# Kernel tuning notes

Hardware: AMD Instinct MI355X
Metric: run time of the kernel (lower is better)

## Reference

```python
import jax, jax.numpy as jnp
import numpy as np

# ---- static config (Phi-3-small layer 0, blocksparse branch) ----
HIDDEN = 4096
N_HEADS = 32
N_KV = 8
HEAD_DIM = HIDDEN // N_HEADS        # 128
Q_PER_KV = N_HEADS // N_KV          # 4
SEQ = 2048
ROPE_BASE = 1000000.0
POS_SCALE = 1.0
SM_SCALE = 1.0 / HEAD_DIM           # mup scaling, multiplier=1.0
BLOCK = 64
LOCAL_BLOCKS = 16
VERT_STRIDE = 8


def _blocksparse_mask(seq_len):
    """Dense [S,S] bool mask realizing the causal blocksparse pattern:
    query block i attends key block j iff j<=i and (i-j < LOCAL_BLOCKS or (j+1) % VERT_STRIDE == 0),
    with elementwise causality inside blocks. Built once in numpy (static)."""
    nb = seq_len // BLOCK
    qb = np.arange(nb)[:, None]
    kb = np.arange(nb)[None, :]
    bmask = (kb <= qb) & ((qb - kb < LOCAL_BLOCKS) | ((kb + 1) % VERT_STRIDE == 0))
    emask = np.kron(bmask, np.ones((BLOCK, BLOCK), dtype=bool))
    i = np.arange(seq_len)
    emask &= i[:, None] >= i[None, :]
    return jnp.asarray(emask)


def _rope(x, cos, sin):
    # x: [B, S, H, D]; cos/sin: [S, D]
    x1, x2 = jnp.split(x, 2, axis=-1)
    rot = jnp.concatenate([-x2, x1], axis=-1)
    return x * cos[None, :, None, :] + rot * sin[None, :, None, :]


def setup_inputs() -> dict:
    key = jax.random.key(0)
    k1, k2, k3, k4, k5 = jax.random.split(key, 5)
    qkv_out = (N_HEADS + 2 * N_KV) * HEAD_DIM  # 6144
    return {
        "hidden_states": jax.random.normal(k1, (1, SEQ, HIDDEN), dtype=jnp.float32),
        "w_qkv": jax.random.normal(k2, (qkv_out, HIDDEN), dtype=jnp.float32) * 0.02,
        "b_qkv": jnp.zeros((qkv_out,), dtype=jnp.float32),
        "w_dense": jax.random.normal(k3, (HIDDEN, HIDDEN), dtype=jnp.float32) * 0.02,
        "b_dense": jnp.zeros((HIDDEN,), dtype=jnp.float32),
    }


def reference(hidden_states, w_qkv, b_qkv, w_dense, b_dense):
    B, S, _ = hidden_states.shape
    # grouped QKV projection: [B,S,(H+2*KV)*D]
    qkv = jnp.einsum("bsh,oh->bso", hidden_states, w_qkv) + b_qkv
    # group layout: (group, q0..q3, k, v) per kv head
    qkv = qkv.reshape(B, S, N_KV, Q_PER_KV + 2, HEAD_DIM)
    q = qkv[:, :, :, :Q_PER_KV].reshape(B, S, N_HEADS, HEAD_DIM)
    k = qkv[:, :, :, Q_PER_KV]   # [B,S,KV,D]
    v = qkv[:, :, :, Q_PER_KV + 1]
    # rotary embeddings (HF rotate-half style)
    inv_freq = 1.0 / (ROPE_BASE ** (jnp.arange(0, HEAD_DIM, 2, dtype=jnp.float32) / HEAD_DIM))
    t = jnp.arange(S, dtype=jnp.float32) * POS_SCALE
    freqs = jnp.outer(t, inv_freq)               # [S, D/2]
    emb = jnp.concatenate([freqs, freqs], axis=-1)
    cos, sin = jnp.cos(emb), jnp.sin(emb)
    q = _rope(q, cos, sin)
    k = _rope(k, cos, sin)
    # GQA: replicate kv heads to match q heads
    k = jnp.repeat(k, Q_PER_KV, axis=2)          # [B,S,H,D]
    v = jnp.repeat(v, Q_PER_KV, axis=2)
    mask = _blocksparse_mask(S)                  # [S,S] bool
    scores = jnp.einsum("bqhd,bkhd->bhqk", q, k) * SM_SCALE
    scores = jnp.where(mask[None, None], scores, jnp.finfo(scores.dtype).min)
    probs = jax.nn.softmax(scores, axis=-1)
    ctx = jnp.einsum("bhqk,bkhd->bqhd", probs, v).reshape(B, S, HIDDEN)
    out = jnp.einsum("bsh,oh->bso", ctx, w_dense) + b_dense
    return out
```

## Files before the change

### kernel.cpp

```cpp
#include <hip/hip_runtime.h>
#include <hip/hip_bf16.h>

#define SEQ 2048
#define HIDDEN 4096
#define NH 32
#define NKV 8
#define HD 128
#define QKV_OUT 6144
#define QSCALE (0.0078125f * 1.4426950408889634f)

typedef __attribute__((ext_vector_type(8))) short bf16x8;
typedef __attribute__((ext_vector_type(4))) float f32x4;
typedef __attribute__((ext_vector_type(16))) float f32x16;

__device__ inline unsigned short f32_bf16(float f) {
  union { float f; unsigned int u; } v; v.f = f;
  unsigned int r = v.u + 0x7FFFu + ((v.u >> 16) & 1u);
  return (unsigned short)(r >> 16);
}
__device__ inline float bf16_f32(unsigned short u) {
  union { unsigned int u; float f; } v; v.u = (unsigned int)u << 16;
  return v.f;
}
__device__ inline unsigned int pk(float a, float b) {
  union { __hip_bfloat162 h; unsigned int u; } t;
  t.h = __float22bfloat162_rn(make_float2(a, b));
  return t.u;
}
__device__ inline void pswap(unsigned int &a, unsigned int &b) {
  auto r = __builtin_amdgcn_permlane32_swap((int)a, (int)b, false, false);
  a = (unsigned int)r[0]; b = (unsigned int)r[1];
}
__device__ inline float xmax32(float v) {
  int x = __builtin_bit_cast(int, v);
  auto r = __builtin_amdgcn_permlane32_swap(x, x, false, false);
  return fmaxf(__builtin_bit_cast(float, (int)r[0]), __builtin_bit_cast(float, (int)r[1]));
}
__device__ inline float xadd32(float v) {
  int x = __builtin_bit_cast(int, v);
  auto r = __builtin_amdgcn_permlane32_swap(x, x, false, false);
  return __builtin_bit_cast(float, (int)r[0]) + __builtin_bit_cast(float, (int)r[1]);
}

__device__ inline void cast8(const float* __restrict__ in, unsigned short* __restrict__ out) {
  float4 a = *reinterpret_cast<const float4*>(in);
  float4 b = *reinterpret_cast<const float4*>(in + 4);
  unsigned short t[8];
  t[0] = f32_bf16(a.x); t[1] = f32_bf16(a.y); t[2] = f32_bf16(a.z); t[3] = f32_bf16(a.w);
  t[4] = f32_bf16(b.x); t[5] = f32_bf16(b.y); t[6] = f32_bf16(b.z); t[7] = f32_bf16(b.w);
  *reinterpret_cast<uint4*>(out) = *reinterpret_cast<uint4*>(t);
}

#define N1 ((size_t)SEQ * HIDDEN / 8)
#define N2 ((size_t)QKV_OUT * HIDDEN / 8)
#define N4 ((size_t)HIDDEN * HIDDEN / 8)
#define N3 ((size_t)SEQ * 64)
__global__ __launch_bounds__(256) void prep(const float* __restrict__ hid,
                                            unsigned short* __restrict__ hid_bf,
                                            const float* __restrict__ wq,
                                            unsigned short* __restrict__ wq_bf,
                                            const float* __restrict__ wd,
                                            unsigned short* __restrict__ wd_bf,
                                            float* __restrict__ ct,
                                            float* __restrict__ st) {
  size_t i = (size_t)blockIdx.x * 256 + threadIdx.x;
  if (i < N1) {
    cast8(hid + i * 8, hid_bf + i * 8);
  } else if (i < N1 + N2) {
    size_t j = (i - N1) * 8;
    cast8(wq + j, wq_bf + j);
  } else if (i < N1 + N2 + N4) {
    size_t j = (i - N1 - N2) * 8;
    cast8(wd + j, wd_bf + j);
  } else {
    size_t j = i - N1 - N2 - N4;
    int s = (int)(j >> 6), d = (int)(j & 63);
    float inv = powf(1.0e6f, -(float)d * (1.0f / 64.0f));
    float f = (float)s * inv;
    ct[j] = cosf(f);
    st[j] = sinf(f);
  }
}

template <int BM, int BN, int CR, int CC, bool OBF>
__global__ __launch_bounds__(512, 2) void gemmG(const unsigned short* __restrict__ A,
                                                const unsigned short* __restrict__ B,
                                                const float* __restrict__ bias,
                                                void* __restrict__ Cp,
                                                int M, int N, int K) {
  constexpr int MQ   = BM / 64;
  constexpr int NREP = BN / 64;
  constexpr int NB0  = (NREP + 1) / 2;
  constexpr int La   = BM / 128;
  constexpr int NB   = BN / 64;
  constexpr int AH   = BM * 64;
  constexpr int SB   = 2 * AH + BN * 128;
  __shared__ __align__(16) char Lds[SB * 2];

  const int tid = threadIdx.x;
  const int wave = tid >> 6, lane = tid & 63;
  const int wr = wave >> 2, wc = wave & 3;
  const int lrow = lane & 15, lgrp = lane >> 4;

  const int ntx = N / BN;
  const int wg0 = blockIdx.x;
  const int xcd = wg0 & 7, w = wg0 >> 3;
  const int cpb = ntx / CC;
  const int band = xcd / cpb, colc = xcd % cpb;
  const int bm = (band * CR + w / CC) * BM;
  const int bn = (colc * CC + w % CC) * BN;

  const int r8 = lane >> 3;
  const int scol = ((lane & 7) ^ r8) * 8;

  const unsigned short* gA[2][La]; int lA[2][La];
#pragma unroll
  for (int u = 0; u < 2; ++u)
#pragma unroll
    for (int j = 0; j < La; ++j) {
      int row = bm + u * (BM / 2) + wave * (BM / 16) + j * 8 + r8;
      gA[u][j] = A + (size_t)row * K + scol;
      lA[u][j] = u * AH + (wave * (BM / 16) + j * 8) * 128;
    }
  const unsigned short* gB[NB]; int lB[NB];
#pragma unroll
  for (int j = 0; j < NB; ++j) {
    int row = bn + wave * (BN / 8) + j * 8 + r8;
    gB[j] = B + (size_t)row * K + scol;
    lB[j] = 2 * AH + (wave * (BN / 8) + j * 8) * 128;
  }

  auto stageA2 = [&](int bufb, int k0) {
#pragma unroll
    for (int u = 0; u < 2; ++u)
#pragma unroll
      for (int j = 0; j < La; ++j)
        __builtin_amdgcn_global_load_lds(
            (const __attribute__((address_space(1))) unsigned int*)(gA[u][j] + k0),
            (__attribute__((address_space(3))) unsigned int*)(Lds + bufb + lA[u][j]), 16, 0, 0);
  };
  auto stageB = [&](int bufb, int k0) {
#pragma unroll
    for (int j = 0; j < NB; ++j)
      __builtin_amdgcn_global_load_lds(
          (const __attribute__((address_space(1))) unsigned int*)(gB[j] + k0),
          (__attribute__((address_space(3))) unsigned int*)(Lds + bufb + lB[j]), 16, 0, 0);
  };

  const int rsw = (lrow & 7) << 4;
  auto aoff = [&](int mh, int m, int ks) {
    int r = mh * (BM / 4) + m * 16 + lrow;
    return wr * AH + r * 128 + ((ks * 64 + lgrp * 16) ^ rsw);
  };
  auto boff = [&](int nf, int ks) {
    int r = wc * (BN / 4) + nf * 16 + lrow;
    return 2 * AH + r * 128 + ((ks * 64 + lgrp * 16) ^ rsw);
  };

  f32x4 acc[2 * MQ][NREP] = {};
  bf16x8 af[MQ][2], bf[NREP][2];

  const int nt = K / 64;
  stageA2(0, 0);
  stageB(0, 0);

  for (int t = 0; t < nt; ++t) {
    const int cur = (t & 1) ? SB : 0;
    const int nxt = cur ^ SB;
    const bool pf = (t + 1) < nt;
    const int k1 = (t + 1) * 64;
    const char* base = Lds + cur;

    if (pf) {
      stageA2(nxt, k1);
      if constexpr (La == 2) asm volatile("s_waitcnt vmcnt(4)" ::: "memory");
      else                   asm volatile("s_waitcnt vmcnt(2)" ::: "memory");
    } else {
      asm volatile("s_waitcnt vmcnt(0)" ::: "memory");
    }
    __builtin_amdgcn_sched_barrier(0);
    __builtin_amdgcn_s_barrier();
    __builtin_amdgcn_sched_barrier(0);
#pragma unroll
    for (int m = 0; m < MQ; ++m)
#pragma unroll
      for (int ks = 0; ks < 2; ++ks)
        af[m][ks] = *reinterpret_cast<const bf16x8*>(base + aoff(0, m, ks));
#pragma unroll
    for (int nf = 0; nf < NB0; ++nf)
#pragma unroll
      for (int ks = 0; ks < 2; ++ks)
        bf[nf][ks] = *reinterpret_cast<const bf16x8*>(base + boff(nf, ks));
    __builtin_amdgcn_s_setprio(1);
#pragma unroll
    for (int m = 0; m < MQ; ++m)
#pragma unroll
      for (int nf = 0; nf < NB0; ++nf)
#pragma unroll
        for (int ks = 0; ks < 2; ++ks)
          acc[m][nf] = __builtin_amdgcn_mfma_f32_16x16x32_bf16(af[m][ks], bf[nf][ks], acc[m][nf], 0, 0, 0);
    __builtin_amdgcn_s_setprio(0);

    if (pf) stageB(nxt, k1);
#pragma unroll
    for (int nf = NB0; nf < NREP; ++nf)
#pragma unroll
      for (int ks = 0; ks < 2; ++ks)
        bf[nf][ks] = *reinterpret_cast<const bf16x8*>(base + boff(nf, ks));
    __builtin_amdgcn_s_setprio(1);
#pragma unroll
    for (int m = 0; m < MQ; ++m)
#pragma unroll
      for (int nf = NB0; nf < NREP; ++nf)
#pragma unroll
        for (int ks = 0; ks < 2; ++ks)
          acc[m][nf] = __builtin_amdgcn_mfma_f32_16x16x32_bf16(af[m][ks], bf[nf][ks], acc[m][nf], 0, 0, 0);
    __builtin_amdgcn_s_setprio(0);

#pragma unroll
    for (int m = 0; m < MQ; ++m)
#pragma unroll
      for (int ks = 0; ks < 2; ++ks)
        af[m][ks] = *reinterpret_cast<const bf16x8*>(base + aoff(1, m, ks));
    __builtin_amdgcn_s_setprio(1);
#pragma unroll
    for (int m = 0; m < MQ; ++m)
#pragma unroll
      for (int nf = 0; nf < NB0; ++nf)
#pragma unroll
        for (int ks = 0; ks < 2; ++ks)
          acc[MQ + m][nf] = __builtin_amdgcn_mfma_f32_16x16x32_bf16(af[m][ks], bf[nf][ks], acc[MQ + m][nf], 0, 0, 0);
    __builtin_amdgcn_s_setprio(0);

    __builtin_amdgcn_s_setprio(1);
#pragma unroll
    for (int m = 0; m < MQ; ++m)
#pragma unroll
      for (int nf = NB0; nf < NREP; ++nf)
#pragma unroll
        for (int ks = 0; ks < 2; ++ks)
          acc[MQ + m][nf] = __builtin_amdgcn_mfma_f32_16x16x32_bf16(af[m][ks], bf[nf][ks], acc[MQ + m][nf], 0, 0, 0);
    __builtin_amdgcn_s_setprio(0);
  }

#pragma unroll
  for (int ni = 0; ni < NREP; ++ni) {
    int col = bn + wc * (BN / 4) + ni * 16 + lrow;
    float bv = bias[col];
#pragma unroll
    for (int mi = 0; mi < 2 * MQ; ++mi)
#pragma unroll
      for (int r = 0; r < 4; ++r) {
        int row = bm + wr * (BM / 2) + mi * 16 + lgrp * 4 + r;
        if constexpr (OBF)
          ((unsigned short*)Cp)[(size_t)row * N + col] = f32_bf16(acc[mi][ni][r] + bv);
        else
          ((float*)Cp)[(size_t)row * N + col] = acc[mi][ni][r] + bv;
      }
  }
}

__global__ __launch_bounds__(256) void rope_split(const unsigned short* __restrict__ qkvb,
                                                  const float* __restrict__ ct,
                                                  const float* __restrict__ st,
                                                  unsigned short* __restrict__ Q,
                                                  unsigned short* __restrict__ Kh,
                                                  unsigned short* __restrict__ Vt) {
  int b = blockIdx.x;
  if (b < 5120) {
    int t = b * 256 + threadIdx.x;
    int d8 = (t & 15) * 8;
    int q = t >> 4;
    int s = q / 40;
    int slotg = q - s * 40;
    int g = slotg / 5, slot = slotg - g * 5;
    const unsigned short* base = qkvb + (size_t)s * QKV_OUT + g * 768 + slot * 128;
    bf16x8 x8 = *reinterpret_cast<const bf16x8*>(base + d8);
    bf16x8 r8 = *reinterpret_cast<const bf16x8*>(base + (d8 ^ 64));
    float4 c0 = *reinterpret_cast<const float4*>(ct + s * 64 + (d8 & 63));
    float4 c1 = *reinterpret_cast<const float4*>(ct + s * 64 + (d8 & 63) + 4);
    float4 s0 = *reinterpret_cast<const float4*>(st + s * 64 + (d8 & 63));
    float4 s1 = *reinterpret_cast<const float4*>(st + s * 64 + (d8 & 63) + 4);
    float cc[8] = {c0.x, c0.y, c0.z, c0.w, c1.x, c1.y, c1.z, c1.w};
    float ss[8] = {s0.x, s0.y, s0.z, s0.w, s1.x, s1.y, s1.z, s1.w};
    float sgn = (d8 < 64) ? -1.0f : 1.0f;
    float sc = (slot < 4) ? QSCALE : 1.0f;
    unsigned short o[8];
#pragma unroll
    for (int i = 0; i < 8; ++i) {
      float x = bf16_f32((unsigned short)x8[i]);
      float r = bf16_f32((unsigned short)r8[i]) * sgn;
      o[i] = f32_bf16((x * cc[i] + r * ss[i]) * sc);
    }
    unsigned short* dst = (slot < 4)
        ? Q + ((size_t)(g * 4 + slot) * SEQ + s) * HD + d8
        : Kh + ((size_t)g * SEQ + s) * HD + d8;
    *reinterpret_cast<uint4*>(dst) = *reinterpret_cast<uint4*>(o);
  } else {
    int t2 = (b - 5120) * 256 + threadIdx.x;
    int d = t2 & 127;
    int rest = t2 >> 7;
    int g = rest & 7;
    int s0 = (rest >> 3) * 8;
    const unsigned short* src = qkvb + (size_t)s0 * QKV_OUT + g * 768 + 640 + d;
    unsigned short o[8];
#pragma unroll
    for (int i = 0; i < 8; ++i) o[i] = src[(size_t)i * QKV_OUT];
    *reinterpret_cast<uint4*>(&Vt[((size_t)g * HD + d) * SEQ + s0]) =
        *reinterpret_cast<uint4*>(o);
  }
}

__device__ inline int nextj(int x, int qb) {
  if (x > qb) return -1;
  if (qb - x < 16) return x;
  int v = (x & ~7) + 7;
  int w = qb - 15;
  return v < w ? v : w;
}

__global__ __launch_bounds__(256, 2) void attn32(const unsigned short* __restrict__ Q,
                                                 const unsigned short* __restrict__ Kh,
                                                 const unsigned short* __restrict__ Vt,
                                                 unsigned short* __restrict__ ctx) {
  const int g = blockIdx.x;
  const int y = (int)gridDim.y - 1 - (int)blockIdx.y;
  const int qb = y >> 1, half = y & 1;
  const int Q0 = y * 32;
  const int tid = threadIdx.x;
  const int wave = tid >> 6;
  const int h = g * 4 + wave;
  const int lane = tid & 63;
  const int l31 = lane & 31, hi = lane >> 5;

  __shared__ __align__(16) char Lds[65536];

  auto stage = [&](int bufb, int j) {
#pragma unroll
    for (int i = 0; i < 4; ++i) {
      int row = i * 16 + (tid >> 4);
      const unsigned short* src =
          Kh + ((size_t)(g * SEQ + j * 64 + row)) * HD + ((tid & 15) ^ (row & 15)) * 8;
      __builtin_amdgcn_global_load_lds(
          (const __attribute__((address_space(1))) unsigned int*)src,
          (__attribute__((address_space(3))) unsigned int*)(Lds + bufb + i * 4096 + (tid >> 6) * 1024),
          16, 0, 0);
    }
#pragma unroll
    for (int i = 0; i < 4; ++i) {
      int row = i * 32 + (tid >> 3);
      const unsigned short* src =
          Vt + ((size_t)(g * HD + row)) * SEQ + j * 64 + ((tid & 7) ^ (row & 7)) * 8;
      __builtin_amdgcn_global_load_lds(
          (const __attribute__((address_space(1))) unsigned int*)src,
          (__attribute__((address_space(3))) unsigned int*)(Lds + bufb + 16384 + i * 4096 + (tid >> 6) * 1024),
          16, 0, 0);
    }
  };

  bf16x8 qf[8];
  const unsigned short* qbase = Q + ((size_t)h * SEQ + Q0 + l31) * HD;
#pragma unroll
  for (int kk = 0; kk < 8; ++kk)
    qf[kk] = *reinterpret_cast<const bf16x8*>(qbase + kk * 16 + hi * 8);

  f32x16 ot[4] = {};
  float mrow = -1e30f, lsum = 0.f;

  const int kswz = l31 & 15;
  const int vswz = l31 & 7;

  int j = nextj(0, qb);
  int cur = 0;
  stage(0, j);
  asm volatile("s_waitcnt vmcnt(0)" ::: "memory");
  __builtin_amdgcn_sched_barrier(0);
  __builtin_amdgcn_s_barrier();
  __builtin_amdgcn_sched_barrier(0);

  while (true) {
    const int jn = (j < qb) ? nextj(j + 1, qb) : -1;
    if (jn >= 0) stage(cur ^ 32768, jn);

    const char* kb = Lds + cur;
    const char* vb = Lds + cur + 16384;
    const bool diag = (j == qb);
    const bool short_blk = diag && (half == 0);

    f32x16 st[2] = {};
    __builtin_amdgcn_s_setprio(1);
#pragma unroll
    for (int kk = 0; kk < 8; ++kk) {
      bf16x8 k0 = *reinterpret_cast<const bf16x8*>(
          kb + (size_t)l31 * 256 + (((2 * kk + hi) ^ kswz) * 16));
      st[0] = __builtin_amdgcn_mfma_f32_32x32x16_bf16(k0, qf[kk], st[0], 0, 0, 0);
      if (!short_blk) {
        bf16x8 k1 = *reinterpret_cast<const bf16x8*>(
            kb + (size_t)(32 + l31) * 256 + (((2 * kk + hi) ^ kswz) * 16));
        st[1] = __builtin_amdgcn_mfma_f32_32x32x16_bf16(k1, qf[kk], st[1], 0, 0, 0);
      }
    }
    __builtin_amdgcn_s_setprio(0);

    if (diag) {
      int qrel = half * 32 + l31;
#pragma unroll
      for (int kt = 0; kt < 2; ++kt)
#pragma unroll
        for (int r = 0; r < 16; ++r) {
          int krel = kt * 32 + (r & 3) + 8 * (r >> 2) + 4 * hi;
          if (krel > qrel) st[kt][r] = -1e30f;
        }
    }

    float t16[16];
#pragma unroll
    for (int r = 0; r < 16; ++r) t16[r] = fmaxf(st[0][r], st[1][r]);
#pragma unroll
    for (int sft = 8; sft >= 1; sft >>= 1)
#pragma unroll
      for (int r = 0; r < sft; ++r) t16[r] = fmaxf(t16[r], t16[r + sft]);
    float vm = xmax32(t16[0]);

    if (!__all(vm - mrow <= 8.0f)) {
      float nm = fmaxf(mrow, vm);
      float corr = __builtin_amdgcn_exp2f(mrow - nm);
      lsum *= corr;
#pragma unroll
      for (int dt = 0; dt < 4; ++dt)
#pragma unroll
        for (int r = 0; r < 16; ++r) ot[dt][r] *= corr;
      mrow = nm;
    }

    float s4[4] = {0.f, 0.f, 0.f, 0.f};
#pragma unroll
    for (int kt = 0; kt < 2; ++kt)
#pragma unroll
      for (int r = 0; r < 16; ++r) {
        float p = __builtin_amdgcn_exp2f(st[kt][r] - mrow);
        st[kt][r] = p;
        s4[r & 3] += p;
      }
    lsum += xadd32((s4[0] + s4[1]) + (s4[2] + s4[3]));

    bf16x8 pb[4];
#pragma unroll
    for (int s = 0; s < 4; ++s) {
      int kt = s >> 1, g0 = (s & 1) * 2, g1 = g0 + 1;
      unsigned int a0 = pk(st[kt][4 * g0 + 0], st[kt][4 * g0 + 1]);
      unsigned int a1 = pk(st[kt][4 * g0 + 2], st[kt][4 * g0 + 3]);
      unsigned int b0 = pk(st[kt][4 * g1 + 0], st[kt][4 * g1 + 1]);
      unsigned int b1 = pk(st[kt][4 * g1 + 2], st[kt][4 * g1 + 3]);
      pswap(a0, b0);
      pswap(a1, b1);
      union { unsigned int u[4]; bf16x8 v; } t;
      t.u[0] = a0; t.u[1] = a1; t.u[2] = b0; t.u[3] = b1;
      pb[s] = t.v;
    }

    const int smax = short_blk ? 2 : 4;
    __builtin_amdgcn_s_setprio(1);
#pragma unroll
    for (int dt = 0; dt < 4; ++dt) {
      const char* vrow = vb + (size_t)(dt * 32 + l31) * 128;
#pragma unroll
      for (int s = 0; s < 4; ++s)
        if (s < smax)
          ot[dt] = __builtin_amdgcn_mfma_f32_32x32x16_bf16(
              *reinterpret_cast<const bf16x8*>(vrow + (((2 * s + hi) ^ vswz) * 16)),
              pb[s], ot[dt], 0, 0, 0);
    }
    __builtin_amdgcn_s_setprio(0);

    if (jn < 0) break;
    asm volatile("s_waitcnt vmcnt(0)" ::: "memory");
    __builtin_amdgcn_sched_barrier(0);
    __builtin_amdgcn_s_barrier();
    __builtin_amdgcn_sched_barrier(0);
    j = jn;
    cur ^= 32768;
  }

  __syncthreads();
  char* W = Lds + wave * 8192;
  float inv = 1.0f / lsum;
  const int swz = (l31 & 7) << 4;
#pragma unroll
  for (int dt = 0; dt < 4; ++dt)
#pragma unroll
    for (int gg = 0; gg < 4; ++gg) {
      unsigned int u0 = pk(ot[dt][4 * gg + 0] * inv, ot[dt][4 * gg + 1] * inv);
      unsigned int u1 = pk(ot[dt][4 * gg + 2] * inv, ot[dt][4 * gg + 3] * inv);
      int off = (dt * 64 + gg * 16 + hi * 8) ^ swz;
      *reinterpret_cast<uint2*>(W + l31 * 256 + off) = make_uint2(u0, u1);
    }
#pragma unroll
  for (int i = 0; i < 8; ++i) {
    int row = lane >> 1;
    int t = (lane & 1) * 8 + i;
    bf16x8 vv = *reinterpret_cast<const bf16x8*>(
        W + row * 256 + ((t * 16) ^ ((row & 7) << 4)));
    *reinterpret_cast<bf16x8*>(&ctx[(size_t)(Q0 + row) * HIDDEN + h * HD + t * 8]) = vv;
  }
}

extern "C" void kernel_launch(void* const* d_in, const int* in_sizes, int n_in,
                              void* d_out, int out_size, void* d_ws, size_t ws_size,
                              hipStream_t stream) {
  const float* hidden  = (const float*)d_in[0];
  const float* w_qkv   = (const float*)d_in[1];
  const float* b_qkv   = (const float*)d_in[2];
  const float* w_dense = (const float*)d_in[3];
  const float* b_dense = (const float*)d_in[4];
  float* out = (float*)d_out;

  char* p = (char*)d_ws;
  unsigned short* hid_bf  = (unsigned short*)p; p += (size_t)SEQ * HIDDEN * 2;
  unsigned short* wqkv_bf = (unsigned short*)p; p += (size_t)QKV_OUT * HIDDEN * 2;
  unsigned short* wd_bf   = (unsigned short*)p; p += (size_t)HIDDEN * HIDDEN * 2;
  unsigned short* qkvb    = (unsigned short*)p; p += (size_t)SEQ * QKV_OUT * 2;
  unsigned short* Qb      = (unsigned short*)p; p += (size_t)NH * SEQ * HD * 2;
  unsigned short* Kb      = (unsigned short*)p; p += (size_t)NKV * SEQ * HD * 2;
  unsigned short* Vt      = (unsigned short*)p; p += (size_t)NKV * HD * SEQ * 2;
  float* ct               = (float*)p;          p += (size_t)SEQ * 64 * 4;
  float* st               = (float*)p;          p += (size_t)SEQ * 64 * 4;
  unsigned short* ctx = hid_bf;

  const int prep_blocks = (int)((N1 + N2 + N4 + N3 + 255) / 256);
  prep<<<prep_blocks, 256, 0, stream>>>(hidden, hid_bf, w_qkv, wqkv_bf,
                                        w_dense, wd_bf, ct, st);

  gemmG<256, 192, 4, 8, true>
      <<<dim3((SEQ / 256) * (QKV_OUT / 192)), 512, 0, stream>>>(
          hid_bf, wqkv_bf, b_qkv, qkvb, SEQ, QKV_OUT, HIDDEN);
  rope_split<<<5120 + 1024, 256, 0, stream>>>(qkvb, ct, st, Qb, Kb, Vt);
  attn32<<<dim3(NKV, SEQ / 32), 256, 0, stream>>>(Qb, Kb, Vt, ctx);
  gemmG<128, 256, 8, 4, false>
      <<<dim3((SEQ / 128) * (HIDDEN / 256)), 512, 0, stream>>>(
          ctx, wd_bf, b_dense, out, SEQ, HIDDEN, HIDDEN);
}
```

Before: 269.3 us.

## Add triple-buffered LDS pipeline and configurable wave layout to bf16 GEMM

The GEMM template gains parameters for the wave-grid shape (RW rows of waves) and the number of LDS buffers. The dense output projection switches to three buffers with prefetch distance two, so global-to-LDS loads have more time in flight before they are consumed. The QKV projection switches to a 4x2 wave grid, which changes how many A and B fragments each wave loads and reuses. Three buffers of about 48 KB each make LDS use much larger, which likely limits the dense GEMM to one workgroup per CU and can cost latency hiding.

```diff
diff --git a/kernel.cpp b/kernel.cpp
--- a/kernel.cpp
+++ b/kernel.cpp
@@ -82,24 +82,25 @@
   }
 }
 
-template <int BM, int BN, int CR, int CC, bool OBF>
+template <int BM, int BN, int RW, int NBUF, int CR, int CC, bool OBF>
 __global__ __launch_bounds__(512, 2) void gemmG(const unsigned short* __restrict__ A,
                                                 const unsigned short* __restrict__ B,
                                                 const float* __restrict__ bias,
                                                 void* __restrict__ Cp,
                                                 int M, int N, int K) {
-  constexpr int MQ   = BM / 64;
-  constexpr int NREP = BN / 64;
+  constexpr int CW   = 8 / RW;
+  constexpr int MQ   = BM / (32 * RW);
+  constexpr int NREP = BN / (16 * CW);
   constexpr int NB0  = (NREP + 1) / 2;
   constexpr int La   = BM / 128;
   constexpr int NB   = BN / 64;
   constexpr int AH   = BM * 64;
   constexpr int SB   = 2 * AH + BN * 128;
-  __shared__ __align__(16) char Lds[SB * 2];
+  __shared__ __align__(16) char Lds[SB * NBUF];
 
   const int tid = threadIdx.x;
   const int wave = tid >> 6, lane = tid & 63;
-  const int wr = wave >> 2, wc = wave & 3;
+  const int wr = wave / CW, wc = wave % CW;
   const int lrow = lane & 15, lgrp = lane >> 4;
 
   const int ntx = N / BN;
@@ -149,11 +150,12 @@
 
   const int rsw = (lrow & 7) << 4;
   auto aoff = [&](int mh, int m, int ks) {
-    int r = mh * (BM / 4) + m * 16 + lrow;
-    return wr * AH + r * 128 + ((ks * 64 + lgrp * 16) ^ rsw);
+    int r = wr * (BM / RW) + mh * (BM / (2 * RW)) + m * 16 + lrow;
+    int u = r / (BM / 2), rr = r % (BM / 2);
+    return u * AH + rr * 128 + ((ks * 64 + lgrp * 16) ^ rsw);
   };
   auto boff = [&](int nf, int ks) {
-    int r = wc * (BN / 4) + nf * 16 + lrow;
+    int r = wc * (BN / CW) + nf * 16 + lrow;
     return 2 * AH + r * 128 + ((ks * 64 + lgrp * 16) ^ rsw);
   };
 
@@ -163,24 +165,37 @@
   const int nt = K / 64;
   stageA2(0, 0);
   stageB(0, 0);
-
+  if constexpr (NBUF == 3) {
+    stageA2(SB, 64);
+    stageB(SB, 64);
+  }
+
+  int bcur = 0;
   for (int t = 0; t < nt; ++t) {
-    const int cur = (t & 1) ? SB : 0;
-    const int nxt = cur ^ SB;
-    const bool pf = (t + 1) < nt;
-    const int k1 = (t + 1) * 64;
+    const int cur = bcur * SB;
+    const int nx1 = (bcur + 1 < NBUF ? bcur + 1 : bcur + 1 - NBUF) * SB;
+    const int nx2 = (bcur + 2 < NBUF ? bcur + 2 : bcur + 2 - NBUF) * SB;
+    const bool pf1 = (t + 1) < nt, pf2 = (t + 2) < nt;
     const char* base = Lds + cur;
 
-    if (pf) {
-      stageA2(nxt, k1);
-      if constexpr (La == 2) asm volatile("s_waitcnt vmcnt(4)" ::: "memory");
-      else                   asm volatile("s_waitcnt vmcnt(2)" ::: "memory");
+    if constexpr (NBUF == 2) {
+      if (pf1) {
+        stageA2(nx1, (t + 1) * 64);
+        if constexpr (La == 2) asm volatile("s_waitcnt vmcnt(4)" ::: "memory");
+        else                   asm volatile("s_waitcnt vmcnt(2)" ::: "memory");
+      } else {
+        asm volatile("s_waitcnt vmcnt(0)" ::: "memory");
+      }
     } else {
-      asm volatile("s_waitcnt vmcnt(0)" ::: "memory");
+      if (pf1) asm volatile("s_waitcnt vmcnt(6)" ::: "memory");
+      else     asm volatile("s_waitcnt vmcnt(0)" ::: "memory");
     }
     __builtin_amdgcn_sched_barrier(0);
     __builtin_amdgcn_s_barrier();
     __builtin_amdgcn_sched_barrier(0);
+    if constexpr (NBUF == 3) {
+      if (pf2) stageA2(nx2, (t + 2) * 64);
+    }
 #pragma unroll
     for (int m = 0; m < MQ; ++m)
 #pragma unroll
@@ -201,7 +216,8 @@
           acc[m][nf] = __builtin_amdgcn_mfma_f32_16x16x32_bf16(af[m][ks], bf[nf][ks], acc[m][nf], 0, 0, 0);
     __builtin_amdgcn_s_setprio(0);
 
-    if (pf) stageB(nxt, k1);
+    if constexpr (NBUF == 2) { if (pf1) stageB(nx1, (t + 1) * 64); }
+    else                     { if (pf2) stageB(nx2, (t + 2) * 64); }
 #pragma unroll
     for (int nf = NB0; nf < NREP; ++nf)
 #pragma unroll
@@ -241,17 +257,19 @@
         for (int ks = 0; ks < 2; ++ks)
           acc[MQ + m][nf] = __builtin_amdgcn_mfma_f32_16x16x32_bf16(af[m][ks], bf[nf][ks], acc[MQ + m][nf], 0, 0, 0);
     __builtin_amdgcn_s_setprio(0);
+
+    bcur = (bcur + 1 < NBUF) ? bcur + 1 : 0;
   }
 
 #pragma unroll
   for (int ni = 0; ni < NREP; ++ni) {
-    int col = bn + wc * (BN / 4) + ni * 16 + lrow;
+    int col = bn + wc * (BN / CW) + ni * 16 + lrow;
     float bv = bias[col];
 #pragma unroll
     for (int mi = 0; mi < 2 * MQ; ++mi)
 #pragma unroll
       for (int r = 0; r < 4; ++r) {
-        int row = bm + wr * (BM / 2) + mi * 16 + lgrp * 4 + r;
+        int row = bm + wr * (BM / RW) + mi * 16 + lgrp * 4 + r;
         if constexpr (OBF)
           ((unsigned short*)Cp)[(size_t)row * N + col] = f32_bf16(acc[mi][ni][r] + bv);
         else
@@ -531,12 +549,12 @@
   prep<<<prep_blocks, 256, 0, stream>>>(hidden, hid_bf, w_qkv, wqkv_bf,
                                         w_dense, wd_bf, ct, st);
 
-  gemmG<256, 192, 4, 8, true>
+  gemmG<256, 192, 4, 2, 4, 8, true>
       <<<dim3((SEQ / 256) * (QKV_OUT / 192)), 512, 0, stream>>>(
           hid_bf, wqkv_bf, b_qkv, qkvb, SEQ, QKV_OUT, HIDDEN);
   rope_split<<<5120 + 1024, 256, 0, stream>>>(qkvb, ct, st, Qb, Kb, Vt);
   attn32<<<dim3(NKV, SEQ / 32), 256, 0, stream>>>(Qb, Kb, Vt, ctx);
-  gemmG<128, 256, 8, 4, false>
+  gemmG<128, 256, 2, 3, 8, 4, false>
       <<<dim3((SEQ / 128) * (HIDDEN / 256)), 512, 0, stream>>>(
           ctx, wd_bf, b_dense, out, SEQ, HIDDEN, HIDDEN);
 }
```

Measured after the change: 267.0 us. Within noise of the previous version (-0.8%).
